# Kernel tuning notes

Hardware: AMD Instinct MI355X
Metric: run time of the kernel (lower is better)

Reference implementation:

```python
import jax, jax.numpy as jnp
import numpy as np

N, H, W, K = 8, 512, 512, 1
NF = 100000  # faces per mesh
D = 8        # attribute channels


def setup_inputs() -> dict:
    key = jax.random.key(0)
    k1, k2, k3 = jax.random.split(key, 3)
    pix_to_face = jax.random.randint(k1, (N, H, W, K), -1 * (N * NF) // 4, N * NF, dtype=jnp.int64)
    pix_to_face = jnp.where(pix_to_face < 0, jnp.int64(-1), pix_to_face)
    # barycentric coords: positive, sum to 1 over last dim (as emitted by rasterizer)
    b = jax.random.uniform(k2, (N, H, W, K, 3), dtype=jnp.float32, minval=1e-3, maxval=1.0)
    bary_coords = b / jnp.sum(b, axis=-1, keepdims=True)
    attributes = jax.random.normal(k3, (N, NF, 3, D), dtype=jnp.float32)
    return {"pix_to_face": pix_to_face, "bary_coords": bary_coords, "attributes": attributes}


def reference(pix_to_face, bary_coords, attributes):
    # attributes: [N, NF, 3, D] -> packed [N*NF, 3, D]
    n, h, w, k, _ = bary_coords.shape
    d = attributes.shape[-1]
    attr = attributes.reshape(-1, 3, d)
    mask = pix_to_face == -1                      # [N,H,W,K]
    idx = jnp.where(mask, 0, pix_to_face)         # clamp invalid to 0
    pixel_face_vals = attr[idx]                   # gather -> [N,H,W,K,3,D]
    pixel_vals = jnp.einsum('nhwkc,nhwkcd->nhwkd', bary_coords, pixel_face_vals)
    pixel_vals = jnp.where(mask[..., None], 0.0, pixel_vals)
    vismask = (~mask).astype(pixel_vals.dtype)    # [N,H,W,K]
    out = jnp.transpose(pixel_vals[:, :, :, 0], (0, 3, 1, 2))   # [N,D,H,W]
    out = jnp.concatenate([out, vismask[:, :, :, 0][:, None]], axis=1)  # [N,D+1,H,W]
    return out
```

## Files before the change

kernel.cpp:

```cpp
#include <hip/hip_runtime.h>

#define NN 8
#define HH 512
#define WW 512
#define DD 8

constexpr int HW   = HH * WW;
constexpr int NPIX = NN * HW;

__global__ __launch_bounds__(256) void interp_face_attrs(
    const int*   __restrict__ p2f,
    const float* __restrict__ bary,
    const float* __restrict__ attr,
    float*       __restrict__ out)
{
    int i = blockIdx.x * blockDim.x + threadIdx.x;
    if (i >= NPIX) return;

    int f = p2f[i];
    int n = i >> 18;
    int p = i & (HW - 1);

    float* ob = out + (size_t)n * (DD + 1) * HW + p;

    if (f < 0) {
        #pragma unroll
        for (int d = 0; d < DD + 1; ++d)
            ob[(size_t)d * HW] = 0.0f;
        return;
    }

    size_t bi = (size_t)i * 3;
    float b0 = bary[bi + 0];
    float b1 = bary[bi + 1];
    float b2 = bary[bi + 2];

    const float4* a = (const float4*)(attr + (size_t)f * 24);
    float4 v00 = a[0];
    float4 v01 = a[1];
    float4 v10 = a[2];
    float4 v11 = a[3];
    float4 v20 = a[4];
    float4 v21 = a[5];

    float o0 = b0 * v00.x + b1 * v10.x + b2 * v20.x;
    float o1 = b0 * v00.y + b1 * v10.y + b2 * v20.y;
    float o2 = b0 * v00.z + b1 * v10.z + b2 * v20.z;
    float o3 = b0 * v00.w + b1 * v10.w + b2 * v20.w;
    float o4 = b0 * v01.x + b1 * v11.x + b2 * v21.x;
    float o5 = b0 * v01.y + b1 * v11.y + b2 * v21.y;
    float o6 = b0 * v01.z + b1 * v11.z + b2 * v21.z;
    float o7 = b0 * v01.w + b1 * v11.w + b2 * v21.w;

    ob[0 * (size_t)HW] = o0;
    ob[1 * (size_t)HW] = o1;
    ob[2 * (size_t)HW] = o2;
    ob[3 * (size_t)HW] = o3;
    ob[4 * (size_t)HW] = o4;
    ob[5 * (size_t)HW] = o5;
    ob[6 * (size_t)HW] = o6;
    ob[7 * (size_t)HW] = o7;
    ob[8 * (size_t)HW] = 1.0f;
}

extern "C" void kernel_launch(void* const* d_in, const int* in_sizes, int n_in,
                              void* d_out, int out_size, void* d_ws, size_t ws_size,
                              hipStream_t stream) {
    const int*   p2f  = (const int*)d_in[0];
    const float* bary = (const float*)d_in[1];
    const float* attr = (const float*)d_in[2];
    float*       out  = (float*)d_out;

    const int block = 256;
    const int grid  = (NPIX + block - 1) / block;
    interp_face_attrs<<<grid, block, 0, stream>>>(p2f, bary, attr, out);
}
```

Baseline: 186.8 us.

## Gather face attributes cooperatively through shared memory with nontemporal output stores

Each block first stages face indices in LDS. Its threads then jointly fetch the 96-byte attribute rows so that neighbouring lanes read neighbouring float4 chunks of the same face, instead of each thread pulling six float4s for its own face. Chunks go into a padded LDS array and are read back per pixel for a vectorized barycentric blend. The branch for invalid pixels is removed by zeroing their weights, and outputs are written with nontemporal stores. This adds two barriers and LDS traffic, and invalid pixels now also gather face 0.

```diff
diff --git a/kernel.cpp b/kernel.cpp
--- a/kernel.cpp
+++ b/kernel.cpp
@@ -7,60 +7,70 @@
 
 constexpr int HW   = HH * WW;
 constexpr int NPIX = NN * HW;
+constexpr int PPB  = 256;
+constexpr int CST  = PPB + 4;
 
-__global__ __launch_bounds__(256) void interp_face_attrs(
+typedef float v4f __attribute__((ext_vector_type(4)));
+
+__global__ __launch_bounds__(256) void interp_coop(
     const int*   __restrict__ p2f,
     const float* __restrict__ bary,
     const float* __restrict__ attr,
     float*       __restrict__ out)
 {
-    int i = blockIdx.x * blockDim.x + threadIdx.x;
-    if (i >= NPIX) return;
+    __shared__ int fIdx[PPB];
+    __shared__ v4f chunks[6 * CST];
+
+    const int t = threadIdx.x;
+    const int i = blockIdx.x * PPB + t;
 
     int f = p2f[i];
-    int n = i >> 18;
-    int p = i & (HW - 1);
-
-    float* ob = out + (size_t)n * (DD + 1) * HW + p;
-
-    if (f < 0) {
-        #pragma unroll
-        for (int d = 0; d < DD + 1; ++d)
-            ob[(size_t)d * HW] = 0.0f;
-        return;
-    }
+    bool valid = f >= 0;
+    fIdx[t] = valid ? f : 0;
 
     size_t bi = (size_t)i * 3;
     float b0 = bary[bi + 0];
     float b1 = bary[bi + 1];
     float b2 = bary[bi + 2];
+    if (!valid) { b0 = 0.0f; b1 = 0.0f; b2 = 0.0f; }
 
-    const float4* a = (const float4*)(attr + (size_t)f * 24);
-    float4 v00 = a[0];
-    float4 v01 = a[1];
-    float4 v10 = a[2];
-    float4 v11 = a[3];
-    float4 v20 = a[4];
-    float4 v21 = a[5];
+    __syncthreads();
 
-    float o0 = b0 * v00.x + b1 * v10.x + b2 * v20.x;
-    float o1 = b0 * v00.y + b1 * v10.y + b2 * v20.y;
-    float o2 = b0 * v00.z + b1 * v10.z + b2 * v20.z;
-    float o3 = b0 * v00.w + b1 * v10.w + b2 * v20.w;
-    float o4 = b0 * v01.x + b1 * v11.x + b2 * v21.x;
-    float o5 = b0 * v01.y + b1 * v11.y + b2 * v21.y;
-    float o6 = b0 * v01.z + b1 * v11.z + b2 * v21.z;
-    float o7 = b0 * v01.w + b1 * v11.w + b2 * v21.w;
+    const v4f* ap = (const v4f*)attr;
+    #pragma unroll
+    for (int j = 0; j < 6; ++j) {
+        int w = j * PPB + t;
+        int p = w / 6;
+        int c = w - p * 6;
+        int ff = fIdx[p];
+        chunks[c * CST + p] = ap[(size_t)ff * 6 + c];
+    }
 
-    ob[0 * (size_t)HW] = o0;
-    ob[1 * (size_t)HW] = o1;
-    ob[2 * (size_t)HW] = o2;
-    ob[3 * (size_t)HW] = o3;
-    ob[4 * (size_t)HW] = o4;
-    ob[5 * (size_t)HW] = o5;
-    ob[6 * (size_t)HW] = o6;
-    ob[7 * (size_t)HW] = o7;
-    ob[8 * (size_t)HW] = 1.0f;
+    __syncthreads();
+
+    v4f x0 = chunks[0 * CST + t];
+    v4f x1 = chunks[1 * CST + t];
+    v4f y0 = chunks[2 * CST + t];
+    v4f y1 = chunks[3 * CST + t];
+    v4f z0 = chunks[4 * CST + t];
+    v4f z1 = chunks[5 * CST + t];
+
+    v4f lo = b0 * x0 + b1 * y0 + b2 * z0;
+    v4f hi = b0 * x1 + b1 * y1 + b2 * z1;
+
+    int n = i >> 18;
+    int p = i & (HW - 1);
+    float* ob = out + (size_t)n * (DD + 1) * HW + p;
+
+    __builtin_nontemporal_store(lo.x, ob + 0 * (size_t)HW);
+    __builtin_nontemporal_store(lo.y, ob + 1 * (size_t)HW);
+    __builtin_nontemporal_store(lo.z, ob + 2 * (size_t)HW);
+    __builtin_nontemporal_store(lo.w, ob + 3 * (size_t)HW);
+    __builtin_nontemporal_store(hi.x, ob + 4 * (size_t)HW);
+    __builtin_nontemporal_store(hi.y, ob + 5 * (size_t)HW);
+    __builtin_nontemporal_store(hi.z, ob + 6 * (size_t)HW);
+    __builtin_nontemporal_store(hi.w, ob + 7 * (size_t)HW);
+    __builtin_nontemporal_store(valid ? 1.0f : 0.0f, ob + 8 * (size_t)HW);
 }
 
 extern "C" void kernel_launch(void* const* d_in, const int* in_sizes, int n_in,
@@ -71,7 +81,6 @@
     const float* attr = (const float*)d_in[2];
     float*       out  = (float*)d_out;
 
-    const int block = 256;
-    const int grid  = (NPIX + block - 1) / block;
-    interp_face_attrs<<<grid, block, 0, stream>>>(p2f, bary, attr, out);
+    const int grid = NPIX / PPB;
+    interp_coop<<<grid, PPB, 0, stream>>>(p2f, bary, attr, out);
 }
```

Result: faster. 182.4 us (median of 2 runs) (-2.3%).

## Process four pixels per thread with vectorized nontemporal loads and stores

Applied to the files above, without the earlier changes.

Each thread now handles four consecutive pixels. It loads face indices and barycentrics as 128-bit vectors and writes each output channel as a float4, using nontemporal hints on the streaming loads and stores. Empty pixels are handled without a branch: the index is clamped to 0 and the weights are zeroed, so every lane gathers. This is meant to cut the number of memory instructions and improve coalescing. In exchange it adds wasted gathers of face 0 for empty pixels, higher register pressure, and fewer threads in flight to hide gather latency.

```diff
diff --git a/kernel.cpp b/kernel.cpp
--- a/kernel.cpp
+++ b/kernel.cpp
@@ -5,62 +5,71 @@
 #define WW 512
 #define DD 8
 
-constexpr int HW   = HH * WW;
-constexpr int NPIX = NN * HW;
+constexpr int HW    = HH * WW;
+constexpr int NPIX  = NN * HW;
+constexpr int NQUAD = NPIX / 4;
 
-__global__ __launch_bounds__(256) void interp_face_attrs(
+typedef float v4f __attribute__((ext_vector_type(4)));
+typedef int   v4i __attribute__((ext_vector_type(4)));
+
+__global__ __launch_bounds__(256) void interp_quad(
     const int*   __restrict__ p2f,
     const float* __restrict__ bary,
     const float* __restrict__ attr,
     float*       __restrict__ out)
 {
-    int i = blockIdx.x * blockDim.x + threadIdx.x;
-    if (i >= NPIX) return;
+    int t = blockIdx.x * blockDim.x + threadIdx.x;
+    if (t >= NQUAD) return;
+    int i0 = t << 2;
 
-    int f = p2f[i];
-    int n = i >> 18;
-    int p = i & (HW - 1);
+    v4i ff = __builtin_nontemporal_load((const v4i*)p2f + t);
+    const v4f* bp = (const v4f*)(bary + 12 * (size_t)t);
+    v4f bA = __builtin_nontemporal_load(bp + 0);
+    v4f bB = __builtin_nontemporal_load(bp + 1);
+    v4f bC = __builtin_nontemporal_load(bp + 2);
 
+    bool vld[4] = { ff.x >= 0, ff.y >= 0, ff.z >= 0, ff.w >= 0 };
+    int  f[4]   = { vld[0] ? ff.x : 0, vld[1] ? ff.y : 0,
+                    vld[2] ? ff.z : 0, vld[3] ? ff.w : 0 };
+    float w0[4] = { bA.x, bA.w, bB.z, bC.y };
+    float w1[4] = { bA.y, bB.x, bB.w, bC.z };
+    float w2[4] = { bA.z, bB.y, bC.x, bC.w };
+    #pragma unroll
+    for (int k = 0; k < 4; ++k)
+        if (!vld[k]) { w0[k] = 0.0f; w1[k] = 0.0f; w2[k] = 0.0f; }
+
+    v4f c[4][6];
+    #pragma unroll
+    for (int k = 0; k < 4; ++k) {
+        const v4f* a = (const v4f*)attr + (size_t)f[k] * 6;
+        #pragma unroll
+        for (int j = 0; j < 6; ++j) c[k][j] = a[j];
+    }
+
+    v4f lo[4], hi[4];
+    #pragma unroll
+    for (int k = 0; k < 4; ++k) {
+        lo[k] = w0[k] * c[k][0] + w1[k] * c[k][2] + w2[k] * c[k][4];
+        hi[k] = w0[k] * c[k][1] + w1[k] * c[k][3] + w2[k] * c[k][5];
+    }
+
+    int n = i0 >> 18;
+    int p = i0 & (HW - 1);
     float* ob = out + (size_t)n * (DD + 1) * HW + p;
 
-    if (f < 0) {
-        #pragma unroll
-        for (int d = 0; d < DD + 1; ++d)
-            ob[(size_t)d * HW] = 0.0f;
-        return;
+    #pragma unroll
+    for (int d = 0; d < 4; ++d) {
+        v4f v = { lo[0][d], lo[1][d], lo[2][d], lo[3][d] };
+        __builtin_nontemporal_store(v, (v4f*)(ob + (size_t)d * HW));
     }
-
-    size_t bi = (size_t)i * 3;
-    float b0 = bary[bi + 0];
-    float b1 = bary[bi + 1];
-    float b2 = bary[bi + 2];
-
-    const float4* a = (const float4*)(attr + (size_t)f * 24);
-    float4 v00 = a[0];
-    float4 v01 = a[1];
-    float4 v10 = a[2];
-    float4 v11 = a[3];
-    float4 v20 = a[4];
-    float4 v21 = a[5];
-
-    float o0 = b0 * v00.x + b1 * v10.x + b2 * v20.x;
-    float o1 = b0 * v00.y + b1 * v10.y + b2 * v20.y;
-    float o2 = b0 * v00.z + b1 * v10.z + b2 * v20.z;
-    float o3 = b0 * v00.w + b1 * v10.w + b2 * v20.w;
-    float o4 = b0 * v01.x + b1 * v11.x + b2 * v21.x;
-    float o5 = b0 * v01.y + b1 * v11.y + b2 * v21.y;
-    float o6 = b0 * v01.z + b1 * v11.z + b2 * v21.z;
-    float o7 = b0 * v01.w + b1 * v11.w + b2 * v21.w;
-
-    ob[0 * (size_t)HW] = o0;
-    ob[1 * (size_t)HW] = o1;
-    ob[2 * (size_t)HW] = o2;
-    ob[3 * (size_t)HW] = o3;
-    ob[4 * (size_t)HW] = o4;
-    ob[5 * (size_t)HW] = o5;
-    ob[6 * (size_t)HW] = o6;
-    ob[7 * (size_t)HW] = o7;
-    ob[8 * (size_t)HW] = 1.0f;
+    #pragma unroll
+    for (int d = 0; d < 4; ++d) {
+        v4f v = { hi[0][d], hi[1][d], hi[2][d], hi[3][d] };
+        __builtin_nontemporal_store(v, (v4f*)(ob + (size_t)(d + 4) * HW));
+    }
+    v4f vis = { vld[0] ? 1.0f : 0.0f, vld[1] ? 1.0f : 0.0f,
+                vld[2] ? 1.0f : 0.0f, vld[3] ? 1.0f : 0.0f };
+    __builtin_nontemporal_store(vis, (v4f*)(ob + (size_t)DD * HW));
 }
 
 extern "C" void kernel_launch(void* const* d_in, const int* in_sizes, int n_in,
@@ -72,6 +81,6 @@
     float*       out  = (float*)d_out;
 
     const int block = 256;
-    const int grid  = (NPIX + block - 1) / block;
-    interp_face_attrs<<<grid, block, 0, stream>>>(p2f, bary, attr, out);
+    const int grid  = (NQUAD + block - 1) / block;
+    interp_quad<<<grid, block, 0, stream>>>(p2f, bary, attr, out);
 }
```

Result: slower. 204.2 us (+9.3%).
